# Kernel optimization log

Hardware: AMD Instinct MI355X
Metric: run time of the kernel (lower is better)

## Reference

```python
import jax, jax.numpy as jnp
import numpy as np
import math

HEAD_DIM = 64           # d_model // n_heads // 2
N_HEADS = 8
LAMBDA_INIT = 0.8 - 0.6 * math.exp(-0.3 * 6)  # depth=6
EPS = 1e-5


def setup_inputs() -> dict:
    key = jax.random.key(0)
    ks = jax.random.split(key, 8)
    B, T, S = 2, 2048, 2048
    return {
        "queries": jax.random.normal(ks[0], (B, 2 * N_HEADS, T, HEAD_DIM), jnp.float32),
        "keys": jax.random.normal(ks[1], (B, 2 * N_HEADS, S, HEAD_DIM), jnp.float32),
        "values": jax.random.normal(ks[2], (B, N_HEADS, S, 2 * HEAD_DIM), jnp.float32),
        "lambda_q1": 0.02 * jax.random.normal(ks[3], (HEAD_DIM,), jnp.float32),
        "lambda_k1": 0.02 * jax.random.normal(ks[4], (HEAD_DIM,), jnp.float32),
        "lambda_q2": 0.02 * jax.random.normal(ks[5], (HEAD_DIM,), jnp.float32),
        "lambda_k2": 0.02 * jax.random.normal(ks[6], (HEAD_DIM,), jnp.float32),
        "subln_weight": jnp.ones((2 * HEAD_DIM,), jnp.float32),
        "tgt_len": 2048,
        "src_len": 2048,
        "attn_mask": jnp.zeros((1,), jnp.bool_),
    }


def reference(queries, keys, values, lambda_q1, lambda_k1, lambda_q2, lambda_k2,
              subln_weight, tgt_len, src_len, attn_mask):
    B = queries.shape[0]
    scaling = HEAD_DIM ** -0.5
    q = queries * scaling
    # [B, 2H, T, S]
    attn_w = jnp.einsum('bhtd,bhsd->bhts', q, keys)
    attn_w = jax.nn.softmax(attn_w.astype(jnp.float32), axis=-1).astype(queries.dtype)
    lam1 = jnp.exp(jnp.sum(lambda_q1 * lambda_k1))
    lam2 = jnp.exp(jnp.sum(lambda_q2 * lambda_k2))
    lam_full = lam1 - lam2 + LAMBDA_INIT
    attn_w = attn_w.reshape(B, N_HEADS, 2, tgt_len, src_len)
    attn_w = attn_w[:, :, 0] - lam_full * attn_w[:, :, 1]   # [B, H, T, S]
    attn = jnp.einsum('bhts,bhse->bhte', attn_w, values)    # [B, H, T, 2*HEAD_DIM]
    # RMSNorm over last dim
    normed = attn * jax.lax.rsqrt(jnp.mean(jnp.square(attn.astype(jnp.float32)), axis=-1, keepdims=True) + EPS).astype(attn.dtype)
    normed = normed * subln_weight
    out = normed * (1.0 - LAMBDA_INIT)
    out = out.transpose(0, 2, 1, 3).reshape(B, tgt_len, N_HEADS * 2 * HEAD_DIM)
    return out
```

## Files before the change

kernel.cpp:

```cpp
#include <hip/hip_runtime.h>
#include <math.h>


#define NT    2048
#define D     64
#define DV    128
#define TQ    64
#define TS    32
#define NROUND (NT / (2 * TS))

#define LAMBDA_INIT 0.70082066706704814f
#define OUT_SCALE   0.29917933293295186f
#define QSCALE      0.18033688011112042f

typedef __attribute__((ext_vector_type(8)))  short    short8;
typedef __attribute__((ext_vector_type(4)))  short    short4v;
typedef __attribute__((ext_vector_type(8)))  _Float16 half8;
typedef __attribute__((ext_vector_type(2)))  __fp16   fp16x2;
typedef __attribute__((ext_vector_type(4)))  float    f32x4;
typedef unsigned short u16;
typedef unsigned int   u32;

#define MFMAH(a, b, c)  __builtin_amdgcn_mfma_f32_16x16x32_f16(a, b, c, 0, 0, 0)
#define MFMA16(a, b, c) __builtin_amdgcn_mfma_f32_16x16x32_bf16(a, b, c, 0, 0, 0)

#if __has_builtin(__builtin_amdgcn_exp2f)
#define EXP2F(x) __builtin_amdgcn_exp2f(x)
#else
#define EXP2F(x) exp2f(x)
#endif

union Hu { half8 v; _Float16 e[8]; u16 s[8]; short8 sv; };

__device__ __forceinline__ u16 f2h(float x) {
    Hu u; u.e[0] = (_Float16)x; return u.s[0];
}

__global__ __launch_bounds__(256) void prep_kv(
    const float* __restrict__ Kg, const float* __restrict__ Vg,
    const float* __restrict__ lq1, const float* __restrict__ lk1,
    const float* __restrict__ lq2, const float* __restrict__ lk2,
    u16* __restrict__ Kf, u16* __restrict__ Vf, float* __restrict__ lamw)
{
    __shared__ u16 th[64 * 136];
    const int bid = blockIdx.x;
    const int t   = threadIdx.x;
    if (bid < 1024) {
        const int bh2 = bid >> 5;
        const int tp  = bid & 31;
        {
            const int key = t >> 2;
            const int d0  = (t & 3) * 16;
            const float* src =
                Kg + ((size_t)bh2 * NT + (size_t)tp * 64 + key) * D + d0;
            const float4 x0 = ((const float4*)src)[0];
            const float4 x1 = ((const float4*)src)[1];
            const float4 x2 = ((const float4*)src)[2];
            const float4 x3 = ((const float4*)src)[3];
            Hu a, b;
            a.e[0] = (_Float16)x0.x; a.e[1] = (_Float16)x0.y;
            a.e[2] = (_Float16)x0.z; a.e[3] = (_Float16)x0.w;
            a.e[4] = (_Float16)x1.x; a.e[5] = (_Float16)x1.y;
            a.e[6] = (_Float16)x1.z; a.e[7] = (_Float16)x1.w;
            b.e[0] = (_Float16)x2.x; b.e[1] = (_Float16)x2.y;
            b.e[2] = (_Float16)x2.z; b.e[3] = (_Float16)x2.w;
            b.e[4] = (_Float16)x3.x; b.e[5] = (_Float16)x3.y;
            b.e[6] = (_Float16)x3.z; b.e[7] = (_Float16)x3.w;
            *(short8*)(th + key * 80 + d0)     = a.sv;
            *(short8*)(th + key * 80 + d0 + 8) = b.sv;
        }
        __syncthreads();
        #pragma unroll
        for (int q = 0; q < 2; ++q) {
            const int c    = t * 2 + q;
            const int tt   = c >> 8;
            const int k0   = (c >> 7) & 1;
            const int mt   = (c >> 6) & 1;
            const int lane = c & 63;
            const int qd   = lane >> 4, lcl = lane & 15;
            const short8 o =
                *(const short8*)(th + (tt * 32 + mt * 16 + lcl) * 80 +
                                 k0 * 32 + qd * 8);
            const size_t oc =
                (((size_t)(bh2 * 64 + tp * 2 + tt)) * 4 + k0 * 2 + mt) * 512 +
                lane * 8;
            *(short8*)(Kf + oc) = o;
        }
        return;
    }
    if (bid == 1024) {
        if (t == 0) {
            float t1 = 0.f, t2 = 0.f;
            for (int i = 0; i < D; ++i) {
                t1 = fmaf(lq1[i], lk1[i], t1);
                t2 = fmaf(lq2[i], lk2[i], t2);
            }
            lamw[0] = __expf(t1) - __expf(t2) + LAMBDA_INIT;
        }
        return;
    }
    const int i  = bid - 1025;
    const int bh = i >> 5;
    const int eb = (i >> 4) & 1;
    const int sb = i & 15;
    const size_t vbase = (size_t)bh * NT * DV + (size_t)sb * 128 * DV + eb * 64;
    {
        const int r0 = t >> 4;
        const int c4 = (t & 15) * 4;
        #pragma unroll
        for (int rr = 0; rr < 8; ++rr) {
            const int row = r0 + rr * 16;
            const float4 x = *(const float4*)(Vg + vbase + (size_t)row * DV + c4);
            th[(c4 + 0) * 136 + row] = f2h(x.x);
            th[(c4 + 1) * 136 + row] = f2h(x.y);
            th[(c4 + 2) * 136 + row] = f2h(x.z);
            th[(c4 + 3) * 136 + row] = f2h(x.w);
        }
    }
    __syncthreads();
    #pragma unroll
    for (int q = 0; q < 4; ++q) {
        const int o    = t * 4 + q;
        const int gt   = o >> 8;
        const int ntl  = (o >> 6) & 3;
        const int lane = o & 63;
        const int cq   = lane >> 4, lcl = lane & 15;
        const int el   = ntl * 16 + lcl;
        Hu ov;
        #pragma unroll
        for (int j = 0; j < 8; ++j)
            ov.s[j] = th[el * 136 + gt * 32 + 4 * cq + (j & 3) + 16 * (j >> 2)];
        const size_t oc =
            (((size_t)(bh * 64 + sb * 4 + gt)) * 8 + eb * 4 + ntl) * 512 +
            lane * 8;
        *(short8*)(Vf + oc) = ov.sv;
    }
}

struct SmemE {
    float epi[2][32][132];
    float lbuf[2][2][2][32];
};

__global__ __launch_bounds__(512, 4) void diffattn_mfma13(
    const float* __restrict__ Qg,
    const u16* __restrict__ Kf, const u16* __restrict__ Vf,
    const float* __restrict__ lamw,
    const float* __restrict__ Wg, float* __restrict__ Outg)
{
    __shared__ SmemE sm;

    const int tid    = threadIdx.x;
    const int wv     = tid >> 6;
    const int lane   = tid & 63;
    const int quad   = lane >> 4;
    const int lc     = lane & 15;
    const int stripe = wv & 1;
    const int hh     = (wv >> 1) & 1;
    const int ks     = wv >> 2;
    const int qt     = blockIdx.x;
    const int bh     = blockIdx.y;
    const int b      = bh >> 3, h = bh & 7;

    const int head2b = b * 16 + 2 * h;
    const int bh8    = b * 8 + h;
    const int bh2    = head2b + hh;
    const float lam  = lamw[0];

    half8 qf[2][2];
    {
        const size_t qhead = (size_t)bh2 * NT * D;
        #pragma unroll
        for (int nq = 0; nq < 2; ++nq) {
            const int row = qt * TQ + stripe * 32 + nq * 16 + lc;
            #pragma unroll
            for (int k0 = 0; k0 < 2; ++k0) {
                const int d0 = k0 * 32 + quad * 8;
                const float4 x = *(const float4*)(Qg + qhead + (size_t)row * D + d0);
                const float4 y = *(const float4*)(Qg + qhead + (size_t)row * D + d0 + 4);
                Hu q;
                q.e[0] = (_Float16)(x.x * QSCALE); q.e[1] = (_Float16)(x.y * QSCALE);
                q.e[2] = (_Float16)(x.z * QSCALE); q.e[3] = (_Float16)(x.w * QSCALE);
                q.e[4] = (_Float16)(y.x * QSCALE); q.e[5] = (_Float16)(y.y * QSCALE);
                q.e[6] = (_Float16)(y.z * QSCALE); q.e[7] = (_Float16)(y.w * QSCALE);
                qf[nq][k0] = q.v;
            }
        }
    }

    f32x4 O_[2][8];
    #pragma unroll
    for (int nq = 0; nq < 2; ++nq)
        #pragma unroll
        for (int nt = 0; nt < 8; ++nt) O_[nq][nt] = (f32x4){0.f, 0.f, 0.f, 0.f};
    float lac[2] = {0.f, 0.f};

    const u32 kbase = (u32)(bh2 * 64) * 2048 + (u32)(lane * 8);
    const u32 vbase = (u32)(bh8 * 64) * 4096 + (u32)(lane * 8);

    const fp16x2 ones = {(__fp16)1.f, (__fp16)1.f};
    const f32x4  z4   = {0.f, 0.f, 0.f, 0.f};

    for (int r = 0; r < NROUND; ++r) {
        const u32 t_ = (u32)(2 * r + ks);
        const u16* kp = Kf + kbase + t_ * 2048;
        const u16* vp = Vf + vbase + t_ * 4096;

        half8 kfr[2][2];
        #pragma unroll
        for (int k0 = 0; k0 < 2; ++k0)
            #pragma unroll
            for (int mt = 0; mt < 2; ++mt)
                kfr[k0][mt] = *(const half8*)(kp + (k0 * 2 + mt) * 512);

        f32x4 sf[2][2];
        #pragma unroll
        for (int mt = 0; mt < 2; ++mt)
            #pragma unroll
            for (int nq = 0; nq < 2; ++nq)
                sf[mt][nq] = MFMAH(kfr[0][mt], qf[nq][0], z4);
        #pragma unroll
        for (int mt = 0; mt < 2; ++mt)
            #pragma unroll
            for (int nq = 0; nq < 2; ++nq)
                sf[mt][nq] = MFMAH(kfr[1][mt], qf[nq][1], sf[mt][nq]);

        half8 a8[2];
        #pragma unroll
        for (int nq = 0; nq < 2; ++nq) {
            union { half8 v; fp16x2 h[4]; } a;
            float ls = lac[nq];
            #pragma unroll
            for (int mt = 0; mt < 2; ++mt)
                #pragma unroll
                for (int ip = 0; ip < 2; ++ip) {
                    const float p0 = EXP2F(sf[mt][nq][2 * ip]);
                    const float p1 = EXP2F(sf[mt][nq][2 * ip + 1]);
                    const fp16x2 h2 = __builtin_amdgcn_cvt_pkrtz(p0, p1);
                    a.h[mt * 2 + ip] = h2;
                    ls = __builtin_amdgcn_fdot2(h2, ones, ls, false);
                }
            lac[nq] = ls;
            a8[nq] = a.v;
        }

        #pragma unroll
        for (int g = 0; g < 2; ++g) {
            half8 vfr[4];
            #pragma unroll
            for (int n = 0; n < 4; ++n)
                vfr[n] = *(const half8*)(vp + (g * 4 + n) * 512);
            #pragma unroll
            for (int n = 0; n < 4; ++n)
                #pragma unroll
                for (int nq = 0; nq < 2; ++nq)
                    O_[nq][g * 4 + n] = MFMAH(a8[nq], vfr[n], O_[nq][g * 4 + n]);
        }
    }

    {
        float s0 = lac[0], s1 = lac[1];
        s0 += __shfl_xor(s0, 16); s0 += __shfl_xor(s0, 32);
        s1 += __shfl_xor(s1, 16); s1 += __shfl_xor(s1, 32);
        if (quad == 0) {
            sm.lbuf[hh][ks][stripe][lc]      = s0;
            sm.lbuf[hh][ks][stripe][16 + lc] = s1;
        }
    }
    __syncthreads();
    float coef[2][4];
    #pragma unroll
    for (int nq = 0; nq < 2; ++nq)
        #pragma unroll
        for (int i = 0; i < 4; ++i) {
            const int row = nq * 16 + quad * 4 + i;
            const float lt = sm.lbuf[hh][0][stripe][row] +
                             sm.lbuf[hh][1][stripe][row];
            coef[nq][i] = (hh == 0) ? (1.f / lt) : (-lam / lt);
        }
    __syncthreads();
    const int pid = hh * 2 + ks;
    #pragma unroll
    for (int p = 0; p < 4; ++p) {
        if (pid == p) {
            #pragma unroll
            for (int nq = 0; nq < 2; ++nq)
                #pragma unroll
                for (int i = 0; i < 4; ++i) {
                    const int row = nq * 16 + quad * 4 + i;
                    #pragma unroll
                    for (int nt = 0; nt < 8; ++nt) {
                        const int col = nt * 16 + lc;
                        const float v = O_[nq][nt][i] * coef[nq][i];
                        if (p == 0) sm.epi[stripe][row][col] = v;
                        else        sm.epi[stripe][row][col] += v;
                    }
                }
        }
        __syncthreads();
    }
    {
        const int r0 = wv * 8 + (lane >> 3);
        const int st = r0 >> 5, ri = r0 & 31;
        const int e0 = (lane & 7) * 16;
        float x[16];
        float ssq = 0.f;
        #pragma unroll
        for (int m = 0; m < 16; m += 4) {
            const float4 t4 = *(const float4*)&sm.epi[st][ri][e0 + m];
            x[m] = t4.x; x[m + 1] = t4.y; x[m + 2] = t4.z; x[m + 3] = t4.w;
            ssq += t4.x * t4.x + t4.y * t4.y + t4.z * t4.z + t4.w * t4.w;
        }
        ssq += __shfl_xor(ssq, 1);
        ssq += __shfl_xor(ssq, 2);
        ssq += __shfl_xor(ssq, 4);
        const float rsq = rsqrtf(ssq * (1.f / 128.f) + 1e-5f) * OUT_SCALE;
        const int rowg = qt * TQ + r0;
        const size_t base =
            ((size_t)b * NT + rowg) * (size_t)(8 * DV) + (size_t)h * DV;
        #pragma unroll
        for (int m = 0; m < 16; m += 4) {
            const float4 w4 = *(const float4*)(Wg + e0 + m);
            float4 o4;
            o4.x = x[m] * rsq * w4.x;
            o4.y = x[m + 1] * rsq * w4.y;
            o4.z = x[m + 2] * rsq * w4.z;
            o4.w = x[m + 3] * rsq * w4.w;
            *(float4*)(Outg + base + e0 + m) = o4;
        }
    }
}

__device__ __forceinline__ unsigned short f2bf(float x) {
    unsigned u = __float_as_uint(x);
    return (unsigned short)((u + 0x7fffu + ((u >> 16) & 1u)) >> 16);
}
__device__ __forceinline__ float bf2f(unsigned short h) {
    return __uint_as_float(((unsigned)h) << 16);
}

struct SmemB {
    union {
        struct {
            short8 kh[2][264];
            short8 kl[2][264];
            short8 vh[516];
            short8 vl[516];
            unsigned short ph[2][2560];
            unsigned short pl[2][2560];
        } L;
        float epi[2][32][132];
    };
};

__global__ __launch_bounds__(256, 2) void diffattn_fb(
    const float* __restrict__ Qg, const float* __restrict__ Kg,
    const float* __restrict__ Vg,
    const float* __restrict__ lq1, const float* __restrict__ lk1,
    const float* __restrict__ lq2, const float* __restrict__ lk2,
    const float* __restrict__ Wg, float* __restrict__ Outg)
{
    __shared__ SmemB sm;
    const int tid = threadIdx.x;
    const int wv = tid >> 6, lane = tid & 63;
    const int quad = lane >> 4, lc = lane & 15;
    const int stripe = wv & 1, hh = wv >> 1;
    const int qt = blockIdx.x, bh = blockIdx.y;
    const int b = bh >> 3, h = bh & 7;
    const size_t koff0 = ((size_t)(b * 16 + 2 * h)) * NT * D;
    const size_t voff  = ((size_t)(b * 8 + h)) * NT * DV;
    float t1 = 0.f, t2 = 0.f;
    for (int i = 0; i < D; ++i) {
        t1 = fmaf(lq1[i], lk1[i], t1);
        t2 = fmaf(lq2[i], lk2[i], t2);
    }
    const float lam = __expf(t1) - __expf(t2) + LAMBDA_INIT;
    short8 qfh[2][2], qfl[2][2];
    {
        const size_t qhead = ((size_t)(b * 16 + 2 * h + hh)) * NT * D;
        #pragma unroll
        for (int mt = 0; mt < 2; ++mt)
            #pragma unroll
            for (int k0 = 0; k0 < 2; ++k0) {
                const int row = qt * TQ + stripe * 32 + mt * 16 + lc;
                const int d0  = k0 * 32 + quad * 8;
                const float4 x = *(const float4*)(Qg + qhead + (size_t)row * D + d0);
                const float4 y = *(const float4*)(Qg + qhead + (size_t)row * D + d0 + 4);
                float f[8] = {x.x, x.y, x.z, x.w, y.x, y.y, y.z, y.w};
                #pragma unroll
                for (int j = 0; j < 8; ++j) {
                    const float v = f[j] * 0.125f;
                    const unsigned short hi = f2bf(v);
                    qfh[mt][k0][j] = (short)hi;
                    qfl[mt][k0][j] = (short)f2bf(v - bf2f(hi));
                }
            }
    }
    f32x4 O_[2][8];
    #pragma unroll
    for (int mt = 0; mt < 2; ++mt)
        #pragma unroll
        for (int nt = 0; nt < 8; ++nt) O_[mt][nt] = (f32x4){0.f, 0.f, 0.f, 0.f};
    float m_[2][4], l_[2][4], a_[2][4];
    #pragma unroll
    for (int mt = 0; mt < 2; ++mt)
        #pragma unroll
        for (int i = 0; i < 4; ++i) { m_[mt][i] = -1e30f; l_[mt][i] = 0.f; }
    const int s_hh = tid >> 7;
    const int s_n  = (tid >> 2) & 31;
    const int s_d0 = (tid & 3) * 16;
    const int s_e0 = tid & 31;
    const int s_s0 = ((tid >> 5) & 7) * 4;
    const int s_sb = s_s0 >> 3;
    const int s_hs = (s_s0 & 4) ? 1 : 0;
    for (int kt = 0; kt < NT / TS; ++kt) {
        const int kb = kt * TS;
        __syncthreads();
        {
            const float* kp = Kg + koff0 + (size_t)s_hh * NT * D +
                              (size_t)(kb + s_n) * D + s_d0;
            const float4 x0 = ((const float4*)kp)[0];
            const float4 x1 = ((const float4*)kp)[1];
            const float4 x2 = ((const float4*)kp)[2];
            const float4 x3 = ((const float4*)kp)[3];
            float f[16] = {x0.x, x0.y, x0.z, x0.w, x1.x, x1.y, x1.z, x1.w,
                           x2.x, x2.y, x2.z, x2.w, x3.x, x3.y, x3.z, x3.w};
            short8 c0h, c0l, c1h, c1l;
            #pragma unroll
            for (int j = 0; j < 8; ++j) {
                unsigned short hi = f2bf(f[j]);
                c0h[j] = (short)hi; c0l[j] = (short)f2bf(f[j] - bf2f(hi));
                hi = f2bf(f[8 + j]);
                c1h[j] = (short)hi; c1l[j] = (short)f2bf(f[8 + j] - bf2f(hi));
            }
            const int db0 = s_d0 >> 3;
            sm.L.kh[s_hh][db0 * 33 + s_n]       = c0h;
            sm.L.kl[s_hh][db0 * 33 + s_n]       = c0l;
            sm.L.kh[s_hh][(db0 + 1) * 33 + s_n] = c1h;
            sm.L.kl[s_hh][(db0 + 1) * 33 + s_n] = c1l;
        }
        {
            #pragma unroll
            for (int j = 0; j < 4; ++j) {
                const int e = s_e0 + 32 * j;
                float f[4];
                #pragma unroll
                for (int i = 0; i < 4; ++i)
                    f[i] = Vg[voff + (size_t)(kb + s_s0 + i) * DV + e];
                short4v hi4, lo4;
                #pragma unroll
                for (int i = 0; i < 4; ++i) {
                    const unsigned short hi = f2bf(f[i]);
                    hi4[i] = (short)hi;
                    lo4[i] = (short)f2bf(f[i] - bf2f(hi));
                }
                ((short4v*)&sm.L.vh[s_sb * 129 + e])[s_hs] = hi4;
                ((short4v*)&sm.L.vl[s_sb * 129 + e])[s_hs] = lo4;
            }
        }
        __syncthreads();
        f32x4 s_f[2][2];
        #pragma unroll
        for (int mt = 0; mt < 2; ++mt)
            #pragma unroll
            for (int nt = 0; nt < 2; ++nt) s_f[mt][nt] = (f32x4){0.f, 0.f, 0.f, 0.f};
        #pragma unroll
        for (int k0 = 0; k0 < 2; ++k0)
            #pragma unroll
            for (int nt = 0; nt < 2; ++nt) {
                const short8 kh = sm.L.kh[hh][(4 * k0 + quad) * 33 + nt * 16 + lc];
                const short8 kl = sm.L.kl[hh][(4 * k0 + quad) * 33 + nt * 16 + lc];
                #pragma unroll
                for (int mt = 0; mt < 2; ++mt) {
                    s_f[mt][nt] = MFMA16(qfh[mt][k0], kh, s_f[mt][nt]);
                    s_f[mt][nt] = MFMA16(qfl[mt][k0], kh, s_f[mt][nt]);
                    s_f[mt][nt] = MFMA16(qfh[mt][k0], kl, s_f[mt][nt]);
                }
            }
        #pragma unroll
        for (int mt = 0; mt < 2; ++mt)
            #pragma unroll
            for (int i = 0; i < 4; ++i) {
                const float v0 = s_f[mt][0][i], v1 = s_f[mt][1][i];
                float mx = fmaxf(v0, v1);
                mx = fmaxf(mx, __shfl_xor(mx, 1));
                mx = fmaxf(mx, __shfl_xor(mx, 2));
                mx = fmaxf(mx, __shfl_xor(mx, 4));
                mx = fmaxf(mx, __shfl_xor(mx, 8));
                const float mn = fmaxf(m_[mt][i], mx);
                const float al = __expf(m_[mt][i] - mn);
                const float p0 = __expf(v0 - mn);
                const float p1 = __expf(v1 - mn);
                float rs = p0 + p1;
                rs += __shfl_xor(rs, 1);
                rs += __shfl_xor(rs, 2);
                rs += __shfl_xor(rs, 4);
                rs += __shfl_xor(rs, 8);
                l_[mt][i] = l_[mt][i] * al + rs;
                m_[mt][i] = mn;
                a_[mt][i] = al;
                const int r = stripe * 32 + mt * 16 + quad * 4 + i;
                const unsigned short h0 = f2bf(p0);
                sm.L.ph[hh][r * 40 + lc]      = h0;
                sm.L.pl[hh][r * 40 + lc]      = f2bf(p0 - bf2f(h0));
                const unsigned short h1 = f2bf(p1);
                sm.L.ph[hh][r * 40 + 16 + lc] = h1;
                sm.L.pl[hh][r * 40 + 16 + lc] = f2bf(p1 - bf2f(h1));
            }
        __syncthreads();
        #pragma unroll
        for (int mt = 0; mt < 2; ++mt)
            #pragma unroll
            for (int nt = 0; nt < 8; ++nt)
                #pragma unroll
                for (int i = 0; i < 4; ++i) O_[mt][nt][i] *= a_[mt][i];
        short8 pah[2], pal[2];
        #pragma unroll
        for (int mt = 0; mt < 2; ++mt) {
            const int r = stripe * 32 + mt * 16 + lc;
            pah[mt] = *(const short8*)&sm.L.ph[hh][r * 40 + quad * 8];
            pal[mt] = *(const short8*)&sm.L.pl[hh][r * 40 + quad * 8];
        }
        #pragma unroll
        for (int nt = 0; nt < 8; ++nt) {
            const short8 vh = sm.L.vh[quad * 129 + nt * 16 + lc];
            const short8 vl = sm.L.vl[quad * 129 + nt * 16 + lc];
            #pragma unroll
            for (int mt = 0; mt < 2; ++mt) {
                O_[mt][nt] = MFMA16(pah[mt], vh, O_[mt][nt]);
                O_[mt][nt] = MFMA16(pal[mt], vh, O_[mt][nt]);
                O_[mt][nt] = MFMA16(pah[mt], vl, O_[mt][nt]);
            }
        }
    }
    __syncthreads();
    if (hh == 1) {
        #pragma unroll
        for (int mt = 0; mt < 2; ++mt)
            #pragma unroll
            for (int i = 0; i < 4; ++i) {
                const float inv = lam / l_[mt][i];
                const int r = mt * 16 + quad * 4 + i;
                #pragma unroll
                for (int nt = 0; nt < 8; ++nt)
                    sm.epi[stripe][r][nt * 16 + lc] = O_[mt][nt][i] * inv;
            }
    }
    __syncthreads();
    if (hh == 0) {
        float wvv[8];
        #pragma unroll
        for (int nt = 0; nt < 8; ++nt) wvv[nt] = Wg[nt * 16 + lc];
        #pragma unroll
        for (int mt = 0; mt < 2; ++mt)
            #pragma unroll
            for (int i = 0; i < 4; ++i) {
                const float inv1 = 1.f / l_[mt][i];
                const int r = mt * 16 + quad * 4 + i;
                float od[8];
                float ss = 0.f;
                #pragma unroll
                for (int nt = 0; nt < 8; ++nt) {
                    od[nt] = O_[mt][nt][i] * inv1 - sm.epi[stripe][r][nt * 16 + lc];
                    ss = fmaf(od[nt], od[nt], ss);
                }
                ss += __shfl_xor(ss, 1);
                ss += __shfl_xor(ss, 2);
                ss += __shfl_xor(ss, 4);
                ss += __shfl_xor(ss, 8);
                const float rsq = rsqrtf(ss * (1.f / 128.f) + 1e-5f) * OUT_SCALE;
                const int rowg = qt * TQ + stripe * 32 + r;
                const size_t base =
                    ((size_t)b * NT + rowg) * (size_t)(8 * DV) + (size_t)h * DV;
                #pragma unroll
                for (int nt = 0; nt < 8; ++nt)
                    Outg[base + nt * 16 + lc] = od[nt] * rsq * wvv[nt];
            }
    }
}

extern "C" void kernel_launch(void* const* d_in, const int* in_sizes, int n_in,
                              void* d_out, int out_size, void* d_ws, size_t ws_size,
                              hipStream_t stream) {
    const float* Q   = (const float*)d_in[0];
    const float* K   = (const float*)d_in[1];
    const float* V   = (const float*)d_in[2];
    const float* lq1 = (const float*)d_in[3];
    const float* lk1 = (const float*)d_in[4];
    const float* lq2 = (const float*)d_in[5];
    const float* lk2 = (const float*)d_in[6];
    const float* W   = (const float*)d_in[7];
    float* Out = (float*)d_out;
    const size_t NEED = 2ull * 4194304ull * sizeof(u16) + 16;
    if (ws_size >= NEED) {
        u16*   Kf   = (u16*)d_ws;
        u16*   Vf   = Kf + 4194304;
        float* lamw = (float*)(Vf + 4194304);
        prep_kv<<<1537, 256, 0, stream>>>(K, V, lq1, lk1, lq2, lk2, Kf, Vf, lamw);
        diffattn_mfma13<<<dim3(NT / TQ, 16), 512, 0, stream>>>(
            Q, Kf, Vf, lamw, W, Out);
    } else {
        diffattn_fb<<<dim3(NT / TQ, 16), 256, 0, stream>>>(
            Q, K, V, lq1, lk1, lq2, lk2, W, Out);
    }
}
```

Baseline: 168.9 us.

## Switch attention to 32x32x16 MFMA with double-buffered LDS staging of K/V

Moves both the QK^T and PV products from 16x16x32 to 32x32x16 f16 MFMA, and changes the prep kernel's K/V fragment layouts to match. K and V tiles are now staged into shared memory with global_load_lds and double-buffered, prefetching the next round while the current one computes, with a block barrier every round. Wave priority is raised around the PV MFMAs. The aim is fewer MFMA issues and better overlap of global loads with compute, at the cost of per-round __syncthreads and larger accumulator register use.

After: 170.0 us. Within noise of the previous version (+0.7%).

```diff
diff --git a/kernel.cpp b/kernel.cpp
--- a/kernel.cpp
+++ b/kernel.cpp
@@ -18,11 +18,12 @@
 typedef __attribute__((ext_vector_type(8)))  _Float16 half8;
 typedef __attribute__((ext_vector_type(2)))  __fp16   fp16x2;
 typedef __attribute__((ext_vector_type(4)))  float    f32x4;
+typedef __attribute__((ext_vector_type(16))) float    f32x16;
 typedef unsigned short u16;
 typedef unsigned int   u32;
 
-#define MFMAH(a, b, c)  __builtin_amdgcn_mfma_f32_16x16x32_f16(a, b, c, 0, 0, 0)
-#define MFMA16(a, b, c) __builtin_amdgcn_mfma_f32_16x16x32_bf16(a, b, c, 0, 0, 0)
+#define MFMA32H(a, b, c) __builtin_amdgcn_mfma_f32_32x32x16_f16(a, b, c, 0, 0, 0)
+#define MFMA16(a, b, c)  __builtin_amdgcn_mfma_f32_16x16x32_bf16(a, b, c, 0, 0, 0)
 
 #if __has_builtin(__builtin_amdgcn_exp2f)
 #define EXP2F(x) __builtin_amdgcn_exp2f(x)
@@ -34,6 +35,12 @@
 
 __device__ __forceinline__ u16 f2h(float x) {
     Hu u; u.e[0] = (_Float16)x; return u.s[0];
+}
+
+__device__ __forceinline__ void glds16(const u16* g, const u16* l) {
+    __builtin_amdgcn_global_load_lds(
+        (const __attribute__((address_space(1))) void*)g,
+        (__attribute__((address_space(3))) void*)l, 16, 0, 0);
 }
 
 __global__ __launch_bounds__(256) void prep_kv(
@@ -74,16 +81,13 @@
         for (int q = 0; q < 2; ++q) {
             const int c    = t * 2 + q;
             const int tt   = c >> 8;
-            const int k0   = (c >> 7) & 1;
-            const int mt   = (c >> 6) & 1;
-            const int lane = c & 63;
-            const int qd   = lane >> 4, lcl = lane & 15;
+            const int i    = (c >> 6) & 3;
+            const int L    = c & 63;
             const short8 o =
-                *(const short8*)(th + (tt * 32 + mt * 16 + lcl) * 80 +
-                                 k0 * 32 + qd * 8);
+                *(const short8*)(th + (tt * 32 + (L & 31)) * 80 +
+                                 i * 16 + (L >> 5) * 8);
             const size_t oc =
-                (((size_t)(bh2 * 64 + tp * 2 + tt)) * 4 + k0 * 2 + mt) * 512 +
-                lane * 8;
+                (((size_t)(bh2 * 64 + tp * 2 + tt)) * 4 + i) * 512 + L * 8;
             *(short8*)(Kf + oc) = o;
         }
         return;
@@ -101,9 +105,9 @@
     }
     const int i  = bid - 1025;
     const int bh = i >> 5;
-    const int eb = (i >> 4) & 1;
+    const int ebH = (i >> 4) & 1;
     const int sb = i & 15;
-    const size_t vbase = (size_t)bh * NT * DV + (size_t)sb * 128 * DV + eb * 64;
+    const size_t vbase = (size_t)bh * NT * DV + (size_t)sb * 128 * DV + ebH * 64;
     {
         const int r0 = t >> 4;
         const int c4 = (t & 15) * 4;
@@ -120,44 +124,52 @@
     __syncthreads();
     #pragma unroll
     for (int q = 0; q < 4; ++q) {
-        const int o    = t * 4 + q;
-        const int gt   = o >> 8;
-        const int ntl  = (o >> 6) & 3;
-        const int lane = o & 63;
-        const int cq   = lane >> 4, lcl = lane & 15;
-        const int el   = ntl * 16 + lcl;
+        const int o   = t * 4 + q;
+        const int gt  = o >> 8;
+        const int elh = (o >> 7) & 1;
+        const int c   = (o >> 6) & 1;
+        const int M   = o & 63;
+        const int el  = elh * 32 + (M & 31);
         Hu ov;
         #pragma unroll
-        for (int j = 0; j < 8; ++j)
-            ov.s[j] = th[el * 136 + gt * 32 + 4 * cq + (j & 3) + 16 * (j >> 2)];
+        for (int j = 0; j < 8; ++j) {
+            const int s = gt * 32 + 16 * c + 4 * (M >> 5) + (j & 3) + 8 * (j >> 2);
+            ov.s[j] = th[el * 136 + s];
+        }
+        const int f = (ebH * 2 + elh) * 2 + c;
         const size_t oc =
-            (((size_t)(bh * 64 + sb * 4 + gt)) * 8 + eb * 4 + ntl) * 512 +
-            lane * 8;
+            (((size_t)(bh * 64 + sb * 4 + gt)) * 8 + f) * 512 + M * 8;
         *(short8*)(Vf + oc) = ov.sv;
     }
 }
 
-struct SmemE {
-    float epi[2][32][132];
-    float lbuf[2][2][2][32];
+struct SmemF {
+    union {
+        short8 c[4096];
+        struct {
+            float epi[2][32][132];
+            float lbuf[2][2][2][32];
+        } e;
+    };
 };
 
-__global__ __launch_bounds__(512, 4) void diffattn_mfma13(
+__global__ __launch_bounds__(512, 4) void diffattn_mfma15(
     const float* __restrict__ Qg,
     const u16* __restrict__ Kf, const u16* __restrict__ Vf,
     const float* __restrict__ lamw,
     const float* __restrict__ Wg, float* __restrict__ Outg)
 {
-    __shared__ SmemE sm;
+    __shared__ SmemF sm;
 
     const int tid    = threadIdx.x;
     const int wv     = tid >> 6;
     const int lane   = tid & 63;
-    const int quad   = lane >> 4;
-    const int lc     = lane & 15;
+    const int hi     = lane >> 5;
+    const int l5     = lane & 31;
     const int stripe = wv & 1;
     const int hh     = (wv >> 1) & 1;
     const int ks     = wv >> 2;
+    const int wig    = wv & 3;
     const int qt     = blockIdx.x;
     const int bh     = blockIdx.y;
     const int b      = bh >> 3, h = bh & 7;
@@ -167,135 +179,143 @@
     const int bh2    = head2b + hh;
     const float lam  = lamw[0];
 
-    half8 qf[2][2];
+    half8 qf[4];
     {
-        const size_t qhead = (size_t)bh2 * NT * D;
-        #pragma unroll
-        for (int nq = 0; nq < 2; ++nq) {
-            const int row = qt * TQ + stripe * 32 + nq * 16 + lc;
-            #pragma unroll
-            for (int k0 = 0; k0 < 2; ++k0) {
-                const int d0 = k0 * 32 + quad * 8;
-                const float4 x = *(const float4*)(Qg + qhead + (size_t)row * D + d0);
-                const float4 y = *(const float4*)(Qg + qhead + (size_t)row * D + d0 + 4);
-                Hu q;
-                q.e[0] = (_Float16)(x.x * QSCALE); q.e[1] = (_Float16)(x.y * QSCALE);
-                q.e[2] = (_Float16)(x.z * QSCALE); q.e[3] = (_Float16)(x.w * QSCALE);
-                q.e[4] = (_Float16)(y.x * QSCALE); q.e[5] = (_Float16)(y.y * QSCALE);
-                q.e[6] = (_Float16)(y.z * QSCALE); q.e[7] = (_Float16)(y.w * QSCALE);
-                qf[nq][k0] = q.v;
-            }
-        }
-    }
-
-    f32x4 O_[2][8];
-    #pragma unroll
-    for (int nq = 0; nq < 2; ++nq)
-        #pragma unroll
-        for (int nt = 0; nt < 8; ++nt) O_[nq][nt] = (f32x4){0.f, 0.f, 0.f, 0.f};
-    float lac[2] = {0.f, 0.f};
-
-    const u32 kbase = (u32)(bh2 * 64) * 2048 + (u32)(lane * 8);
-    const u32 vbase = (u32)(bh8 * 64) * 4096 + (u32)(lane * 8);
+        const int   row   = qt * TQ + stripe * 32 + l5;
+        const float* qrow = Qg + ((size_t)bh2 * NT + row) * D;
+        #pragma unroll
+        for (int i = 0; i < 4; ++i) {
+            const int d0 = i * 16 + hi * 8;
+            const float4 x = *(const float4*)(qrow + d0);
+            const float4 y = *(const float4*)(qrow + d0 + 4);
+            Hu q;
+            q.e[0] = (_Float16)(x.x * QSCALE); q.e[1] = (_Float16)(x.y * QSCALE);
+            q.e[2] = (_Float16)(x.z * QSCALE); q.e[3] = (_Float16)(x.w * QSCALE);
+            q.e[4] = (_Float16)(y.x * QSCALE); q.e[5] = (_Float16)(y.y * QSCALE);
+            q.e[6] = (_Float16)(y.z * QSCALE); q.e[7] = (_Float16)(y.w * QSCALE);
+            qf[i] = q.v;
+        }
+    }
+
+    const f32x16 z16 = {0.f, 0.f, 0.f, 0.f, 0.f, 0.f, 0.f, 0.f,
+                        0.f, 0.f, 0.f, 0.f, 0.f, 0.f, 0.f, 0.f};
+    f32x16 O_[4];
+    #pragma unroll
+    for (int eb = 0; eb < 4; ++eb) O_[eb] = z16;
+    float lac = 0.f;
+
+    u32 kSrc[2], vSrc[2];
+    u32 kDst[2], vDst[2];
+    #pragma unroll
+    for (int t = 0; t < 2; ++t) {
+        const int fk  = wig * 2 + t;
+        const int hhs = fk >> 2;
+        const int ii  = fk & 3;
+        kSrc[t] = (u32)((head2b + hhs) * 64) * 2048 + (u32)(ii * 512 + lane * 8);
+        kDst[t] = (u32)(ks * 8192 + fk * 512);
+        vSrc[t] = (u32)(bh8 * 64) * 4096 + (u32)(fk * 512 + lane * 8);
+        vDst[t] = (u32)(ks * 8192 + 4096 + fk * 512);
+    }
+    const u16* ldsu = (const u16*)&sm.c[0];
+
+    #pragma unroll
+    for (int t = 0; t < 2; ++t) {
+        glds16(Kf + kSrc[t] + (u32)ks * 2048, ldsu + kDst[t]);
+        glds16(Vf + vSrc[t] + (u32)ks * 4096, ldsu + vDst[t]);
+    }
+    __syncthreads();
+
+    u32 kOff[4], vOff[8];
+    #pragma unroll
+    for (int i = 0; i < 4; ++i)
+        kOff[i] = (u32)(ks * 8192 + (hh * 4 + i) * 512 + lane * 8);
+    #pragma unroll
+    for (int f = 0; f < 8; ++f)
+        vOff[f] = (u32)(ks * 8192 + 4096 + f * 512 + lane * 8);
 
     const fp16x2 ones = {(__fp16)1.f, (__fp16)1.f};
-    const f32x4  z4   = {0.f, 0.f, 0.f, 0.f};
 
     for (int r = 0; r < NROUND; ++r) {
-        const u32 t_ = (u32)(2 * r + ks);
-        const u16* kp = Kf + kbase + t_ * 2048;
-        const u16* vp = Vf + vbase + t_ * 4096;
-
-        half8 kfr[2][2];
-        #pragma unroll
-        for (int k0 = 0; k0 < 2; ++k0)
-            #pragma unroll
-            for (int mt = 0; mt < 2; ++mt)
-                kfr[k0][mt] = *(const half8*)(kp + (k0 * 2 + mt) * 512);
-
-        f32x4 sf[2][2];
-        #pragma unroll
-        for (int mt = 0; mt < 2; ++mt)
-            #pragma unroll
-            for (int nq = 0; nq < 2; ++nq)
-                sf[mt][nq] = MFMAH(kfr[0][mt], qf[nq][0], z4);
-        #pragma unroll
-        for (int mt = 0; mt < 2; ++mt)
-            #pragma unroll
-            for (int nq = 0; nq < 2; ++nq)
-                sf[mt][nq] = MFMAH(kfr[1][mt], qf[nq][1], sf[mt][nq]);
-
-        half8 a8[2];
-        #pragma unroll
-        for (int nq = 0; nq < 2; ++nq) {
-            union { half8 v; fp16x2 h[4]; } a;
-            float ls = lac[nq];
-            #pragma unroll
-            for (int mt = 0; mt < 2; ++mt)
-                #pragma unroll
-                for (int ip = 0; ip < 2; ++ip) {
-                    const float p0 = EXP2F(sf[mt][nq][2 * ip]);
-                    const float p1 = EXP2F(sf[mt][nq][2 * ip + 1]);
-                    const fp16x2 h2 = __builtin_amdgcn_cvt_pkrtz(p0, p1);
-                    a.h[mt * 2 + ip] = h2;
-                    ls = __builtin_amdgcn_fdot2(h2, ones, ls, false);
-                }
-            lac[nq] = ls;
-            a8[nq] = a.v;
-        }
-
-        #pragma unroll
-        for (int g = 0; g < 2; ++g) {
-            half8 vfr[4];
-            #pragma unroll
-            for (int n = 0; n < 4; ++n)
-                vfr[n] = *(const half8*)(vp + (g * 4 + n) * 512);
-            #pragma unroll
-            for (int n = 0; n < 4; ++n)
-                #pragma unroll
-                for (int nq = 0; nq < 2; ++nq)
-                    O_[nq][g * 4 + n] = MFMAH(a8[nq], vfr[n], O_[nq][g * 4 + n]);
-        }
+        const u32 bo = ((u32)(r & 1)) << 14;
+
+        if (r < NROUND - 1) {
+            const u32 tn = (u32)(2 * (r + 1) + ks);
+            const u32 ab = ((u32)((r + 1) & 1)) << 14;
+            #pragma unroll
+            for (int t = 0; t < 2; ++t) {
+                glds16(Kf + kSrc[t] + tn * 2048, ldsu + ab + kDst[t]);
+                glds16(Vf + vSrc[t] + tn * 4096, ldsu + ab + vDst[t]);
+            }
+        }
+
+        f32x16 sf;
+        {
+            const half8 ka0 = *(const half8*)(ldsu + bo + kOff[0]);
+            sf = MFMA32H(ka0, qf[0], z16);
+            const half8 ka1 = *(const half8*)(ldsu + bo + kOff[1]);
+            sf = MFMA32H(ka1, qf[1], sf);
+            const half8 ka2 = *(const half8*)(ldsu + bo + kOff[2]);
+            sf = MFMA32H(ka2, qf[2], sf);
+            const half8 ka3 = *(const half8*)(ldsu + bo + kOff[3]);
+            sf = MFMA32H(ka3, qf[3], sf);
+        }
+
+        union { half8 v[2]; fp16x2 h[8]; } a;
+        {
+            float ls = lac;
+            #pragma unroll
+            for (int m = 0; m < 8; ++m) {
+                const float p0 = EXP2F(sf[2 * m]);
+                const float p1 = EXP2F(sf[2 * m + 1]);
+                const fp16x2 h2 = __builtin_amdgcn_cvt_pkrtz(p0, p1);
+                a.h[m] = h2;
+                ls = __builtin_amdgcn_fdot2(h2, ones, ls, false);
+            }
+            lac = ls;
+        }
+
+        __builtin_amdgcn_s_setprio(1);
+        #pragma unroll
+        for (int eb = 0; eb < 4; ++eb) {
+            const half8 v0 = *(const half8*)(ldsu + bo + vOff[eb * 2]);
+            const half8 v1 = *(const half8*)(ldsu + bo + vOff[eb * 2 + 1]);
+            O_[eb] = MFMA32H(a.v[0], v0, O_[eb]);
+            O_[eb] = MFMA32H(a.v[1], v1, O_[eb]);
+        }
+        __builtin_amdgcn_s_setprio(0);
+
+        __syncthreads();
     }
 
     {
-        float s0 = lac[0], s1 = lac[1];
-        s0 += __shfl_xor(s0, 16); s0 += __shfl_xor(s0, 32);
-        s1 += __shfl_xor(s1, 16); s1 += __shfl_xor(s1, 32);
-        if (quad == 0) {
-            sm.lbuf[hh][ks][stripe][lc]      = s0;
-            sm.lbuf[hh][ks][stripe][16 + lc] = s1;
-        }
+        const float s0 = lac + __shfl_xor(lac, 32);
+        if (lane < 32) sm.e.lbuf[hh][ks][stripe][l5] = s0;
     }
     __syncthreads();
-    float coef[2][4];
-    #pragma unroll
-    for (int nq = 0; nq < 2; ++nq)
-        #pragma unroll
-        for (int i = 0; i < 4; ++i) {
-            const int row = nq * 16 + quad * 4 + i;
-            const float lt = sm.lbuf[hh][0][stripe][row] +
-                             sm.lbuf[hh][1][stripe][row];
-            coef[nq][i] = (hh == 0) ? (1.f / lt) : (-lam / lt);
-        }
+    float coef[16];
+    #pragma unroll
+    for (int reg = 0; reg < 16; ++reg) {
+        const int row = (reg & 3) + 8 * (reg >> 2) + 4 * hi;
+        const float lt = sm.e.lbuf[hh][0][stripe][row] +
+                         sm.e.lbuf[hh][1][stripe][row];
+        coef[reg] = (hh == 0) ? (1.f / lt) : (-lam / lt);
+    }
     __syncthreads();
     const int pid = hh * 2 + ks;
     #pragma unroll
     for (int p = 0; p < 4; ++p) {
         if (pid == p) {
             #pragma unroll
-            for (int nq = 0; nq < 2; ++nq)
-                #pragma unroll
-                for (int i = 0; i < 4; ++i) {
-                    const int row = nq * 16 + quad * 4 + i;
-                    #pragma unroll
-                    for (int nt = 0; nt < 8; ++nt) {
-                        const int col = nt * 16 + lc;
-                        const float v = O_[nq][nt][i] * coef[nq][i];
-                        if (p == 0) sm.epi[stripe][row][col] = v;
-                        else        sm.epi[stripe][row][col] += v;
-                    }
+            for (int reg = 0; reg < 16; ++reg) {
+                const int row = (reg & 3) + 8 * (reg >> 2) + 4 * hi;
+                #pragma unroll
+                for (int eb = 0; eb < 4; ++eb) {
+                    const int col = eb * 32 + l5;
+                    const float v = O_[eb][reg] * coef[reg];
+                    if (p == 0) sm.e.epi[stripe][row][col] = v;
+                    else        sm.e.epi[stripe][row][col] += v;
                 }
+            }
         }
         __syncthreads();
     }
@@ -307,7 +327,7 @@
         float ssq = 0.f;
         #pragma unroll
         for (int m = 0; m < 16; m += 4) {
-            const float4 t4 = *(const float4*)&sm.epi[st][ri][e0 + m];
+            const float4 t4 = *(const float4*)&sm.e.epi[st][ri][e0 + m];
             x[m] = t4.x; x[m + 1] = t4.y; x[m + 2] = t4.z; x[m + 3] = t4.w;
             ssq += t4.x * t4.x + t4.y * t4.y + t4.z * t4.z + t4.w * t4.w;
         }
@@ -597,7 +617,7 @@
         u16*   Vf   = Kf + 4194304;
         float* lamw = (float*)(Vf + 4194304);
         prep_kv<<<1537, 256, 0, stream>>>(K, V, lq1, lk1, lq2, lk2, Kf, Vf, lamw);
-        diffattn_mfma13<<<dim3(NT / TQ, 16), 512, 0, stream>>>(
+        diffattn_mfma15<<<dim3(NT / TQ, 16), 512, 0, stream>>>(
             Q, Kf, Vf, lamw, W, Out);
     } else {
         diffattn_fb<<<dim3(NT / TQ, 16), 256, 0, stream>>>(
```
